# Optimization experiments

Measured on AMD Instinct MI355X. Metric: run time of the kernel, lower is better.

Reference implementation:

```python
import jax, jax.numpy as jnp
import numpy as np

B, N = 16, 4096
D_IN, D_OUT, HID, E = 128, 128, 256, 8
SG_HID = 16  # SharedGate hidden fixed at 16 in __init__


def setup_inputs() -> dict:
    key = jax.random.key(0)
    ks = jax.random.split(key, 6)
    s = 0.05
    return {
        "x": jax.random.normal(ks[0], (B, N, D_IN), dtype=jnp.float32),
        "active_experts": jnp.ones((B, E), dtype=jnp.int32),
        # SharedGate: fc1 [16, D_IN], fc2 [D_IN, 16] (torch Linear weight is [out, in])
        "sg_w1": jax.random.normal(ks[1], (SG_HID, D_IN), dtype=jnp.float32) * s,
        "sg_w2": jax.random.normal(ks[2], (D_IN, SG_HID), dtype=jnp.float32) * s,
        # TaskSpecificGate: E linears [1, D_IN] -> stacked [E, D_IN]
        "gate_w": jax.random.normal(ks[3], (E, D_IN), dtype=jnp.float32) * s,
        # Expert MLPs (no bias): fc1 [E, HID, D_IN], fc2 [E, D_OUT, HID]
        "exp_w1": jax.random.normal(ks[4], (E, HID, D_IN), dtype=jnp.float32) * s,
        "exp_w2": jax.random.normal(ks[5], (E, D_OUT, HID), dtype=jnp.float32) * s,
    }


def reference(x, active_experts, sg_w1, sg_w2, gate_w, exp_w1, exp_w2):
    b, n, d_in = x.shape
    xf = x.reshape(-1, d_in)  # [T, D_IN], T = B*N (node-level routing)

    # SharedGate with residual: fc2(relu(fc1(x))) + x
    shared = jnp.maximum(xf @ sg_w1.T, 0.0) @ sg_w2.T + xf  # [T, D_IN]

    # Task-specific gate: per-expert scalar scores, masked softmax over experts
    scores = (shared @ gate_w.T).reshape(b, n, -1)  # [B, N, E]
    mask = active_experts.astype(bool)[:, None, :]  # [B, 1, E]
    masked = jnp.where(mask, scores, -jnp.inf)
    weights = jax.nn.softmax(masked, axis=-1)  # [B, N, E]

    # All experts (dense): batched two-layer MLP per expert
    h = jnp.maximum(jnp.einsum("td,ehd->teh", xf, exp_w1), 0.0)  # [T, E, HID]
    out = jnp.einsum("teh,eoh->teo", h, exp_w2)  # [T, E, D_OUT]
    out_r = out.reshape(b, n, weights.shape[-1], -1)  # [B, N, E, D_OUT]

    # Gate-weighted combine over experts
    output_end = jnp.sum(out_r * weights[..., None], axis=2)  # [B, N, D_OUT]
    aux_loss = jnp.float32(0.0)  # sign=False
    return output_end, aux_loss
```

## Files before the change

### kernel.cpp

```cpp
#include <hip/hip_runtime.h>
#include <hip/hip_bf16.h>


typedef float f32x4 __attribute__((ext_vector_type(4)));
typedef short bf16x8 __attribute__((ext_vector_type(8)));

static __device__ __forceinline__ short f2bs(float f) {
  union { __hip_bfloat16 b; short s; } u;
  u.b = __float2bfloat16(f);
  return u.s;
}

static __device__ __forceinline__ unsigned pk2(float lo, float hi) {
  union { __hip_bfloat162 b; unsigned u; } t;
  t.b = __float22bfloat162_rn(make_float2(lo, hi));
  return t.u;
}


__global__ void prep_kernel(const float* __restrict__ sg_w1,
                            const float* __restrict__ sg_w2,
                            const float* __restrict__ gate_w,
                            const float* __restrict__ exp_w1,
                            const float* __restrict__ exp_w2,
                            short* __restrict__ ws_s) {
  int idx = blockIdx.x * 256 + threadIdx.x;
  if (idx < 262144) {
    int e = idx >> 15, rem = idx & 32767;
    int frag = rem >> 9, lane = (rem >> 3) & 63, j = rem & 7;
    int hid = (frag >> 2) * 16 + (lane & 15);
    int k   = (frag & 3) * 32 + (lane >> 4) * 8 + j;
    ws_s[idx] = f2bs(exp_w1[(e * 256 + hid) * 128 + k]);
  } else if (idx < 524288) {
    int i2 = idx - 262144;
    int e = i2 >> 15, rem = i2 & 32767;
    int frag = rem >> 9, lane = (rem >> 3) & 63, j = rem & 7;
    int lg = lane >> 4, l15 = lane & 15;
    int ks = frag >> 3;
    int oi = frag & 7;
    int o  = oi * 16 + l15;
    int h  = ks * 32 + (j < 4 ? lg * 4 + j : 16 + lg * 4 + (j - 4));
    ws_s[idx] = f2bs(exp_w2[(e * 128 + o) * 256 + h]);
  } else if (idx < 526336) {
    int i3 = idx - 524288;
    int k = i3 >> 9, lane = (i3 >> 3) & 63, j = i3 & 7;
    int lg = lane >> 4, l15 = lane & 15;
    ws_s[idx] = f2bs(sg_w1[l15 * 128 + k * 32 + lg * 8 + j]);
  } else if (idx < 528384) {
    int i4 = idx - 526336;
    int k = i4 >> 9, lane = (i4 >> 3) & 63, j = i4 & 7;
    int lg = lane >> 4, l15 = lane & 15;
    ws_s[idx] = (l15 < 8) ? f2bs(gate_w[l15 * 128 + k * 32 + lg * 8 + j]) : (short)0;
  } else if (idx < 528896) {
    int i5 = idx - 528384;
    int lane = (i5 >> 3) & 63, j = i5 & 7;
    int lg = lane >> 4, l15 = lane & 15;
    int kk = lg * 8 + j;
    if (l15 < 8 && kk < 16) {
      float acc = 0.f;
      for (int d = 0; d < 128; ++d) acc += gate_w[l15 * 128 + d] * sg_w2[d * 16 + kk];
      ws_s[idx] = f2bs(acc);
    } else {
      ws_s[idx] = 0;
    }
  }
}

__global__ __launch_bounds__(512, 2) void moe_kernel(
    const float* __restrict__ x, const int* __restrict__ active,
    const short* __restrict__ ws_s, float* __restrict__ out) {
  __shared__ __align__(16) short Wbuf[2][8192];
  __shared__ short Ul[8][1280];

  const short* W1p  = ws_s;
  const short* W2p  = ws_s + 262144;
  const short* sg1p = ws_s + 524288;
  const short* gwp  = ws_s + 526336;
  const short* gcp  = ws_s + 528384;

  const int tid  = threadIdx.x;
  const int lane = tid & 63;
  const int wid  = tid >> 6;
  const int l15  = lane & 15;
  const int lg   = lane >> 4;
  const int tokw = blockIdx.x * 256 + wid * 32;

  auto stage = [&](int buf, int c) {
    const short* s1 = W1p + (size_t)(c * 8 + wid) * 512 + lane * 8;
    const short* s2 = W2p + (size_t)(c * 8 + wid) * 512 + lane * 8;
    __builtin_amdgcn_global_load_lds(
        (const __attribute__((address_space(1))) void*)s1,
        (__attribute__((address_space(3))) void*)(&Wbuf[buf][wid * 512]),
        16, 0, 0);
    __builtin_amdgcn_global_load_lds(
        (const __attribute__((address_space(1))) void*)s2,
        (__attribute__((address_space(3))) void*)(&Wbuf[buf][4096 + wid * 512]),
        16, 0, 0);
  };

  stage(0, 0);

  short* Ulw = &Ul[wid][0];
  for (int i = lane; i < 640; i += 64) ((int*)Ulw)[i] = 0;

  bf16x8 xf[2][4];
  {
    int trow = tokw + l15;
#pragma unroll
    for (int m = 0; m < 2; ++m) {
      const float* xr = x + (size_t)(trow + m * 16) * 128;
#pragma unroll
      for (int k = 0; k < 4; ++k) {
        int c = k * 32 + lg * 8;
        float4 a = *(const float4*)(xr + c);
        float4 b = *(const float4*)(xr + c + 4);
        bf16x8 v;
        v[0] = f2bs(a.x); v[1] = f2bs(a.y); v[2] = f2bs(a.z); v[3] = f2bs(a.w);
        v[4] = f2bs(b.x); v[5] = f2bs(b.y); v[6] = f2bs(b.z); v[7] = f2bs(b.w);
        xf[m][k] = v;
      }
    }
  }
  __syncthreads();

  f32x4 wreg[2];
  {
    bf16x8 sgf[4], gwf[4];
#pragma unroll
    for (int k = 0; k < 4; ++k) {
      sgf[k] = *(const bf16x8*)(sg1p + k * 512 + lane * 8);
      gwf[k] = *(const bf16x8*)(gwp  + k * 512 + lane * 8);
    }
#pragma unroll
    for (int m = 0; m < 2; ++m) {
      f32x4 acc = {0.f, 0.f, 0.f, 0.f};
#pragma unroll
      for (int k = 0; k < 4; ++k)
        acc = __builtin_amdgcn_mfma_f32_16x16x32_bf16(xf[m][k], sgf[k], acc, 0, 0, 0);
#pragma unroll
      for (int r = 0; r < 4; ++r)
        Ulw[(m * 16 + lg * 4 + r) * 40 + l15] = f2bs(fmaxf(acc[r], 0.f));
    }
    f32x4 sc[2];
#pragma unroll
    for (int m = 0; m < 2; ++m) {
      f32x4 acc = {0.f, 0.f, 0.f, 0.f};
#pragma unroll
      for (int k = 0; k < 4; ++k)
        acc = __builtin_amdgcn_mfma_f32_16x16x32_bf16(xf[m][k], gwf[k], acc, 0, 0, 0);
      sc[m] = acc;
    }
    __syncthreads();
    bf16x8 gcf = *(const bf16x8*)(gcp + lane * 8);
#pragma unroll
    for (int m = 0; m < 2; ++m) {
      bf16x8 uf = *(const bf16x8*)(Ulw + (m * 16 + l15) * 40 + lg * 8);
      sc[m] = __builtin_amdgcn_mfma_f32_16x16x32_bf16(uf, gcf, sc[m], 0, 0, 0);
    }
    int b = tokw >> 12;
    float am = (l15 < 8 && active[b * 8 + l15] != 0) ? 0.f : -3.0e38f;
#pragma unroll
    for (int m = 0; m < 2; ++m) {
      f32x4 w4;
#pragma unroll
      for (int r = 0; r < 4; ++r) {
        float s = sc[m][r] + am;
        float mx = s;
        mx = fmaxf(mx, __shfl_xor(mx, 1));
        mx = fmaxf(mx, __shfl_xor(mx, 2));
        mx = fmaxf(mx, __shfl_xor(mx, 4));
        float p = __expf(s - mx);
        float su = p;
        su += __shfl_xor(su, 1);
        su += __shfl_xor(su, 2);
        su += __shfl_xor(su, 4);
        w4[r] = p / su;
      }
      wreg[m] = w4;
    }
  }

  f32x4 acc2[2][8];
#pragma unroll
  for (int m = 0; m < 2; ++m)
#pragma unroll
    for (int o = 0; o < 8; ++o)
      acc2[m][o] = {0.f, 0.f, 0.f, 0.f};

  for (int e = 0; e < 8; ++e) {
    float wv[2];
    {
      int srcb = ((l15 >> 2) << 4) | e;
      int rp = l15 & 3;
#pragma unroll
      for (int m = 0; m < 2; ++m) {
        float q0 = __shfl(wreg[m][0], srcb), q1 = __shfl(wreg[m][1], srcb);
        float q2 = __shfl(wreg[m][2], srcb), q3 = __shfl(wreg[m][3], srcb);
        float lo = (rp & 1) ? q1 : q0, hi = (rp & 1) ? q3 : q2;
        wv[m] = (rp & 2) ? hi : lo;
      }
    }
#pragma unroll
    for (int ks = 0; ks < 8; ++ks) {
      int c = e * 8 + ks;
      if (c < 63) stage((ks + 1) & 1, c + 1);
      const short* wb = &Wbuf[ks & 1][0];

      bf16x8 Af[8], Bf[8];
#pragma unroll
      for (int i = 0; i < 8; ++i) {
        Af[i] = *(const bf16x8*)(wb + i * 512 + lane * 8);
        Bf[i] = *(const bf16x8*)(wb + 4096 + i * 512 + lane * 8);
      }

      f32x4 a1[2][2];
#pragma unroll
      for (int m = 0; m < 2; ++m)
#pragma unroll
        for (int n = 0; n < 2; ++n) {
          f32x4 acc = {0.f, 0.f, 0.f, 0.f};
#pragma unroll
          for (int kx = 0; kx < 4; ++kx)
            acc = __builtin_amdgcn_mfma_f32_16x16x32_bf16(Af[n * 4 + kx], xf[m][kx], acc, 0, 0, 0);
          a1[m][n] = acc;
        }

      bf16x8 hB[2];
#pragma unroll
      for (int m = 0; m < 2; ++m) {
        float s = wv[m];
        float v0 = fmaxf(a1[m][0][0], 0.f) * s, v1 = fmaxf(a1[m][0][1], 0.f) * s;
        float v2 = fmaxf(a1[m][0][2], 0.f) * s, v3 = fmaxf(a1[m][0][3], 0.f) * s;
        float w0 = fmaxf(a1[m][1][0], 0.f) * s, w1 = fmaxf(a1[m][1][1], 0.f) * s;
        float w2 = fmaxf(a1[m][1][2], 0.f) * s, w3 = fmaxf(a1[m][1][3], 0.f) * s;
        union { unsigned u[4]; bf16x8 v; } hb;
        hb.u[0] = pk2(v0, v1); hb.u[1] = pk2(v2, v3);
        hb.u[2] = pk2(w0, w1); hb.u[3] = pk2(w2, w3);
        hB[m] = hb.v;
      }

#pragma unroll
      for (int o = 0; o < 8; ++o)
#pragma unroll
        for (int m = 0; m < 2; ++m)
          acc2[m][o] = __builtin_amdgcn_mfma_f32_16x16x32_bf16(Bf[o], hB[m], acc2[m][o], 0, 0, 0);

      __syncthreads();
    }
  }

#pragma unroll
  for (int m = 0; m < 2; ++m)
#pragma unroll
    for (int o = 0; o < 8; ++o)
      *(f32x4*)(out + (size_t)(tokw + m * 16 + l15) * 128 + o * 16 + lg * 4) = acc2[m][o];

  if (blockIdx.x == 0 && tid == 0) out[8388608] = 0.0f;
}

extern "C" void kernel_launch(void* const* d_in, const int* in_sizes, int n_in,
                              void* d_out, int out_size, void* d_ws, size_t ws_size,
                              hipStream_t stream) {
  const float* x      = (const float*)d_in[0];
  const int*   act    = (const int*)d_in[1];
  const float* sg_w1  = (const float*)d_in[2];
  const float* sg_w2  = (const float*)d_in[3];
  const float* gate_w = (const float*)d_in[4];
  const float* exp_w1 = (const float*)d_in[5];
  const float* exp_w2 = (const float*)d_in[6];
  short* ws_s = (short*)d_ws;
  float* out = (float*)d_out;

  prep_kernel<<<2066, 256, 0, stream>>>(sg_w1, sg_w2, gate_w, exp_w1, exp_w2, ws_s);
  moe_kernel<<<256, 512, 0, stream>>>(x, act, ws_s, out);
}
```

Before: 91.00 us.

## Halve block size and load W2 fragments directly to registers with double buffering

Blocks shrink from 8 to 4 waves (128 tokens each) and the grid doubles to 512. Only the expert fc1 weights are still staged through LDS via global_load_lds. The fc2 weight fragments are now loaded straight from global memory into ping-pong register arrays, one chunk ahead. This halves LDS use and the LDS read traffic per chunk. In exchange it raises register pressure and makes each wave fetch W2 from L2 independently, doubling global weight traffic per token.

After: 92.59 us. No clear change (+1.7%).

```diff
diff --git a/kernel.cpp b/kernel.cpp
--- a/kernel.cpp
+++ b/kernel.cpp
@@ -66,11 +66,11 @@
   }
 }
 
-__global__ __launch_bounds__(512, 2) void moe_kernel(
+__global__ __launch_bounds__(256, 2) void moe_kernel(
     const float* __restrict__ x, const int* __restrict__ active,
     const short* __restrict__ ws_s, float* __restrict__ out) {
-  __shared__ __align__(16) short Wbuf[2][8192];
-  __shared__ short Ul[8][1280];
+  __shared__ __align__(16) short Abuf[2][4096];
+  __shared__ short Ul[4][1280];
 
   const short* W1p  = ws_s;
   const short* W2p  = ws_s + 262144;
@@ -83,22 +83,27 @@
   const int wid  = tid >> 6;
   const int l15  = lane & 15;
   const int lg   = lane >> 4;
-  const int tokw = blockIdx.x * 256 + wid * 32;
-
-  auto stage = [&](int buf, int c) {
-    const short* s1 = W1p + (size_t)(c * 8 + wid) * 512 + lane * 8;
-    const short* s2 = W2p + (size_t)(c * 8 + wid) * 512 + lane * 8;
-    __builtin_amdgcn_global_load_lds(
-        (const __attribute__((address_space(1))) void*)s1,
-        (__attribute__((address_space(3))) void*)(&Wbuf[buf][wid * 512]),
-        16, 0, 0);
-    __builtin_amdgcn_global_load_lds(
-        (const __attribute__((address_space(1))) void*)s2,
-        (__attribute__((address_space(3))) void*)(&Wbuf[buf][4096 + wid * 512]),
-        16, 0, 0);
+  const int tokw = blockIdx.x * 128 + wid * 32;
+
+  auto stageA = [&](int buf, int c) {
+#pragma unroll
+    for (int t = 0; t < 2; ++t) {
+      int i = wid * 2 + t;
+      const short* s = W1p + ((size_t)c * 8 + i) * 512 + lane * 8;
+      __builtin_amdgcn_global_load_lds(
+          (const __attribute__((address_space(1))) void*)s,
+          (__attribute__((address_space(3))) void*)(&Abuf[buf][i * 512]),
+          16, 0, 0);
+    }
   };
-
-  stage(0, 0);
+  auto loadB = [&](bf16x8 (&B)[8], int c) {
+    const short* p = W2p + (size_t)c * 4096 + lane * 8;
+#pragma unroll
+    for (int oi = 0; oi < 8; ++oi)
+      B[oi] = *(const bf16x8*)(p + oi * 512);
+  };
+
+  stageA(0, 0);
 
   short* Ulw = &Ul[wid][0];
   for (int i = lane; i < 640; i += 64) ((int*)Ulw)[i] = 0;
@@ -187,6 +192,9 @@
     for (int o = 0; o < 8; ++o)
       acc2[m][o] = {0.f, 0.f, 0.f, 0.f};
 
+  bf16x8 Ba[8], Bb[8];
+  loadB(Ba, 0);
+
   for (int e = 0; e < 8; ++e) {
     float wv[2];
     {
@@ -200,18 +208,16 @@
         wv[m] = (rp & 2) ? hi : lo;
       }
     }
-#pragma unroll
-    for (int ks = 0; ks < 8; ++ks) {
-      int c = e * 8 + ks;
-      if (c < 63) stage((ks + 1) & 1, c + 1);
-      const short* wb = &Wbuf[ks & 1][0];
-
-      bf16x8 Af[8], Bf[8];
-#pragma unroll
-      for (int i = 0; i < 8; ++i) {
-        Af[i] = *(const bf16x8*)(wb + i * 512 + lane * 8);
-        Bf[i] = *(const bf16x8*)(wb + 4096 + i * 512 + lane * 8);
-      }
+
+    auto chunk_body = [&](bf16x8 (&Bcur)[8], bf16x8 (&Bnext)[8], int bufA, int c) {
+      if (c < 63) {
+        stageA(bufA ^ 1, c + 1);
+        loadB(Bnext, c + 1);
+      }
+      bf16x8 Af[8];
+#pragma unroll
+      for (int i = 0; i < 8; ++i)
+        Af[i] = *(const bf16x8*)(&Abuf[bufA][i * 512 + lane * 8]);
 
       f32x4 a1[2][2];
 #pragma unroll
@@ -224,28 +230,31 @@
             acc = __builtin_amdgcn_mfma_f32_16x16x32_bf16(Af[n * 4 + kx], xf[m][kx], acc, 0, 0, 0);
           a1[m][n] = acc;
         }
-
       bf16x8 hB[2];
 #pragma unroll
       for (int m = 0; m < 2; ++m) {
         float s = wv[m];
-        float v0 = fmaxf(a1[m][0][0], 0.f) * s, v1 = fmaxf(a1[m][0][1], 0.f) * s;
-        float v2 = fmaxf(a1[m][0][2], 0.f) * s, v3 = fmaxf(a1[m][0][3], 0.f) * s;
-        float w0 = fmaxf(a1[m][1][0], 0.f) * s, w1 = fmaxf(a1[m][1][1], 0.f) * s;
-        float w2 = fmaxf(a1[m][1][2], 0.f) * s, w3 = fmaxf(a1[m][1][3], 0.f) * s;
         union { unsigned u[4]; bf16x8 v; } hb;
-        hb.u[0] = pk2(v0, v1); hb.u[1] = pk2(v2, v3);
-        hb.u[2] = pk2(w0, w1); hb.u[3] = pk2(w2, w3);
+        hb.u[0] = pk2(fmaxf(a1[m][0][0], 0.f) * s, fmaxf(a1[m][0][1], 0.f) * s);
+        hb.u[1] = pk2(fmaxf(a1[m][0][2], 0.f) * s, fmaxf(a1[m][0][3], 0.f) * s);
+        hb.u[2] = pk2(fmaxf(a1[m][1][0], 0.f) * s, fmaxf(a1[m][1][1], 0.f) * s);
+        hb.u[3] = pk2(fmaxf(a1[m][1][2], 0.f) * s, fmaxf(a1[m][1][3], 0.f) * s);
         hB[m] = hb.v;
       }
-
 #pragma unroll
       for (int o = 0; o < 8; ++o)
 #pragma unroll
         for (int m = 0; m < 2; ++m)
-          acc2[m][o] = __builtin_amdgcn_mfma_f32_16x16x32_bf16(Bf[o], hB[m], acc2[m][o], 0, 0, 0);
+          acc2[m][o] = __builtin_amdgcn_mfma_f32_16x16x32_bf16(Bcur[o], hB[m], acc2[m][o], 0, 0, 0);
 
       __syncthreads();
+    };
+
+#pragma unroll
+    for (int kk = 0; kk < 4; ++kk) {
+      int c0 = e * 8 + 2 * kk;
+      chunk_body(Ba, Bb, 0, c0);
+      chunk_body(Bb, Ba, 1, c0 + 1);
     }
   }
 
@@ -272,5 +281,5 @@
   float* out = (float*)d_out;
 
   prep_kernel<<<2066, 256, 0, stream>>>(sg_w1, sg_w2, gate_w, exp_w1, exp_w2, ws_s);
-  moe_kernel<<<256, 512, 0, stream>>>(x, act, ws_s, out);
-}
+  moe_kernel<<<512, 256, 0, stream>>>(x, act, ws_s, out);
+}
```
